# Kernel tuning notes

Measured on AMD Instinct MI355X. Metric: run time of the kernel, lower is better.

The kernel has to match this reference:

```python
import jax, jax.numpy as jnp
import numpy as np

RADIUS = 4  # matches init radius


def _bilinear_sample(v, grid):
    """Faithful F.grid_sample(v, grid, mode='bilinear', align_corners=True, padding_mode='zeros').
    v: (B,C,H,W); grid: (B,Hg,Wg,2) in [-1,1]; grid[...,0]->width(x), grid[...,1]->height(y)."""
    B, C, H, W = v.shape
    Hg, Wg = grid.shape[1], grid.shape[2]
    ix = (grid[..., 0] + 1.0) * 0.5 * (W - 1)
    iy = (grid[..., 1] + 1.0) * 0.5 * (H - 1)
    x0 = jnp.floor(ix); y0 = jnp.floor(iy)
    x1 = x0 + 1.0;      y1 = y0 + 1.0
    wx1 = ix - x0; wx0 = 1.0 - wx1
    wy1 = iy - y0; wy0 = 1.0 - wy1
    v_flat = v.reshape(B, C, H * W)
    out = jnp.zeros((B, C, Hg, Wg), v.dtype)
    for xf, yf, w in ((x0, y0, wx0 * wy0), (x1, y0, wx1 * wy0),
                      (x0, y1, wx0 * wy1), (x1, y1, wx1 * wy1)):
        valid = (xf >= 0) & (xf <= W - 1) & (yf >= 0) & (yf <= H - 1)
        xi = jnp.clip(xf, 0, W - 1).astype(jnp.int32)
        yi = jnp.clip(yf, 0, H - 1).astype(jnp.int32)
        idx = (yi * W + xi).reshape(B, 1, Hg * Wg)
        g = jnp.take_along_axis(v_flat, idx, axis=2).reshape(B, C, Hg, Wg)
        out = out + g * (w * valid)[:, None, :, :]
    return out


def setup_inputs() -> dict:
    key = jax.random.key(0)
    ks = jax.random.split(key, 5)
    B, C, H, W, K = 4, 128, 128, 128, 8
    x = jax.random.normal(ks[0], (B, C, H, W), jnp.float32)
    psf_tbl = jax.random.randint(ks[1], (B, H, W, K, 2), 0, 128)  # absolute pixel anchors
    delta = jax.random.normal(ks[2], (1, 1, 1, K, 2), jnp.float32) * 0.1
    w_qkv = jax.random.normal(ks[3], (3 * C, C), jnp.float32) * (C ** -0.5)  # 1x1 conv, no bias
    w_proj = jax.random.normal(ks[4], (C, C), jnp.float32) * (C ** -0.5)
    return {"x": x, "psf_tbl": psf_tbl, "delta": delta, "w_qkv": w_qkv, "w_proj": w_proj}


def reference(x, psf_tbl, delta, w_qkv, w_proj):
    B, C, H, W = x.shape
    K = psf_tbl.shape[3]
    qkv = jnp.einsum('oc,bchw->bohw', w_qkv, x)  # 1x1 conv to_qkv
    q, k, v = jnp.split(qkv, 3, axis=1)
    offsets = psf_tbl.astype(x.dtype) + jnp.tanh(delta) * RADIUS  # (B,H,W,K,2)
    norm = jnp.array([H - 1, W - 1], x.dtype)
    grid = (offsets / norm * 2.0 - 1.0).reshape(B, H, W * K, 2)
    k_s = _bilinear_sample(k, grid).reshape(B, C, H, W, K)
    v_s = _bilinear_sample(v, grid).reshape(B, C, H, W, K)
    attn = jnp.einsum('bchw,bchwk->bhwk', q, k_s) * (C ** -0.5)
    attn = jax.nn.softmax(attn, axis=-1)  # softmax over K sampled points
    out = jnp.einsum('bhwk,bchwk->bchw', attn, v_s)
    return x + jnp.einsum('oc,bchw->bohw', w_proj, out)
```

## Files before the change

kernel.cpp:

```cpp
#include <hip/hip_runtime.h>

#define HW 16384
#define C 128

typedef __attribute__((ext_vector_type(8))) short short8;
typedef __attribute__((ext_vector_type(4))) float f32x4;
typedef __attribute__((ext_vector_type(2))) float f32x2;
typedef __attribute__((ext_vector_type(16))) int v16i;

__device__ __forceinline__ unsigned short f2bf(float f) {
  union { float f; unsigned u; } v; v.f = f;
  return (unsigned short)((v.u + 0x7fffu + ((v.u >> 16) & 1u)) >> 16);
}
#if __has_builtin(__builtin_amdgcn_cvt_pk_bf16_f32)
typedef __attribute__((ext_vector_type(2))) __bf16 bf16x2;
__device__ __forceinline__ unsigned pk2(float a, float b) {
  union { bf16x2 v; unsigned u; } cv;
  cv.v = __builtin_amdgcn_cvt_pk_bf16_f32(a, b);
  return cv.u;
}
#else
__device__ __forceinline__ unsigned pk2(float a, float b) {
  return (unsigned)f2bf(a) | ((unsigned)f2bf(b) << 16);
}
#endif
__device__ __forceinline__ unsigned short f2bf1(float a) {
  return (unsigned short)(pk2(a, a) & 0xffffu);
}
__device__ __forceinline__ float bflo(unsigned w) {
  union { unsigned u; float f; } v; v.u = w << 16; return v.f;
}
__device__ __forceinline__ float bfhi(unsigned w) {
  union { unsigned u; float f; } v; v.u = w & 0xffff0000u; return v.f;
}
__device__ __forceinline__ float asf(int u) {
  union { int u; float f; } v; v.u = u; return v.f;
}
__device__ __forceinline__ float bf2f(unsigned short h) {
  union { unsigned u; float f; } v; v.u = ((unsigned)h) << 16; return v.f;
}

__global__ __launch_bounds__(128) void k_prep(const float* __restrict__ w_qkv,
                                              const float* __restrict__ w_proj,
                                              const float* __restrict__ delta,
                                              unsigned short* __restrict__ Mt,
                                              unsigned short* __restrict__ Pm,
                                              float* __restrict__ pw,
                                              int* __restrict__ pi) {
  const int bid = blockIdx.x;
  const int t = threadIdx.x;
  if (bid == 256) {
    if (t < 8) {
      float s0 = tanhf(delta[t * 2 + 0]) * 4.0f;
      float s1 = tanhf(delta[t * 2 + 1]) * 4.0f;
      float f0 = floorf(s0), f1 = floorf(s1);
      pi[2 * t + 0] = (int)f0;
      pi[2 * t + 1] = (int)f1;
      float fx = s0 - f0, fy = s1 - f1;
      pw[4 * t + 0] = (1.0f - fx) * (1.0f - fy);
      pw[4 * t + 1] = fx * (1.0f - fy);
      pw[4 * t + 2] = (1.0f - fx) * fy;
      pw[4 * t + 3] = fx * fy;
    }
    return;
  }
  const int R = bid & 127;
  float acc = 0.0f;
  if (bid < 128) {
    const float* wq = w_qkv;
    const float* wk = w_qkv + 128 * 128;
    #pragma unroll 16
    for (int j = 0; j < 128; ++j)
      acc += wk[j * 128 + R] * wq[j * 128 + t];
    acc *= 0.08838834764831845f;
    Mt[R * 128 + (t ^ ((R & 7) << 3))] = f2bf1(acc);
  } else {
    const float* wv = w_qkv + 2 * 128 * 128;
    const float* wp = w_proj + (size_t)R * 128;
    #pragma unroll 16
    for (int j = 0; j < 128; ++j)
      acc += wp[j] * wv[j * 128 + t];
    Pm[R * 128 + (t ^ ((R & 7) << 3))] = f2bf1(acc);
  }
}

__global__ __launch_bounds__(256) void k_qx(const float* __restrict__ x,
                                            const unsigned short* __restrict__ Mt,
                                            unsigned short* __restrict__ qb,
                                            unsigned* __restrict__ xq) {
  __shared__ __align__(16) unsigned char smem[65536];
  unsigned short* Xs = (unsigned short*)smem;
  unsigned short* Ws = (unsigned short*)(smem + 32768);
  const int t = threadIdx.x;
  const int gpix0 = blockIdx.x * 128;
  const int b = gpix0 >> 14;
  const int hw0 = gpix0 & (HW - 1);

  const float* xb = x + (size_t)b * C * HW + hw0;
  #pragma unroll
  for (int i = 0; i < 16; ++i) {
    int linear = i * 256 + t;
    int p = linear & 127;
    int c4 = (linear >> 7) * 4;
    float a0 = xb[(size_t)(c4 + 0) * HW + p];
    float a1 = xb[(size_t)(c4 + 1) * HW + p];
    float a2 = xb[(size_t)(c4 + 2) * HW + p];
    float a3 = xb[(size_t)(c4 + 3) * HW + p];
    int cc = c4 ^ ((p & 7) << 3);
    *(uint2*)&Xs[p * 128 + cc] = make_uint2(pk2(a0, a1), pk2(a2, a3));
  }
  #pragma unroll
  for (int i = 0; i < 8; ++i)
    ((uint4*)Ws)[i * 256 + t] = ((const uint4*)Mt)[i * 256 + t];
  __syncthreads();

  #pragma unroll
  for (int i = 0; i < 8; ++i) {
    int linear = i * 256 + t;
    int c8 = (linear & 15) * 8;
    int prow = linear >> 4;
    uint4 v = *(const uint4*)&Xs[prow * 128 + (c8 ^ ((prow & 7) << 3))];
    *(uint4*)&xq[((size_t)(gpix0 + prow)) * 64 + (c8 >> 1)] = v;
  }

  const int wave = t >> 6, lane = t & 63;
  const int wr = wave >> 1, wc = wave & 1;
  const int rsel = lane & 15, quad = lane >> 4;

  f32x4 acc[4][4];
  #pragma unroll
  for (int mi = 0; mi < 4; ++mi)
    #pragma unroll
    for (int ni = 0; ni < 4; ++ni) acc[mi][ni] = (f32x4){0.f, 0.f, 0.f, 0.f};
  #pragma unroll
  for (int ks = 0; ks < 4; ++ks) {
    const int koff = ks * 32 + quad * 8;
    short8 afr[4], bfr[4];
    #pragma unroll
    for (int mi = 0; mi < 4; ++mi) {
      int r = wr * 64 + mi * 16 + rsel;
      afr[mi] = *(const short8*)&Xs[r * 128 + (koff ^ ((r & 7) << 3))];
    }
    #pragma unroll
    for (int ni = 0; ni < 4; ++ni) {
      int r = wc * 64 + ni * 16 + rsel;
      bfr[ni] = *(const short8*)&Ws[r * 128 + (koff ^ ((r & 7) << 3))];
    }
    #pragma unroll
    for (int mi = 0; mi < 4; ++mi)
      #pragma unroll
      for (int ni = 0; ni < 4; ++ni)
        acc[mi][ni] = __builtin_amdgcn_mfma_f32_16x16x32_bf16(afr[mi], bfr[ni], acc[mi][ni], 0, 0, 0);
  }
  __syncthreads();
  #pragma unroll
  for (int mi = 0; mi < 4; ++mi)
    #pragma unroll
    for (int ni = 0; ni < 4; ++ni)
      #pragma unroll
      for (int r = 0; r < 4; ++r) {
        int p = wr * 64 + mi * 16 + quad * 4 + r;
        int ch = wc * 64 + ni * 16 + rsel;
        Xs[p * 128 + (ch ^ ((p & 7) << 3))] = f2bf1(acc[mi][ni][r]);
      }
  __syncthreads();
  #pragma unroll
  for (int i = 0; i < 8; ++i) {
    int linear = i * 256 + t;
    int c8 = (linear & 15) * 8;
    int prow = linear >> 4;
    uint4 v = *(const uint4*)&Xs[prow * 128 + (c8 ^ ((prow & 7) << 3))];
    *(uint4*)(qb + (size_t)(gpix0 + prow) * C + c8) = v;
  }
}

__global__ __launch_bounds__(256) void k_attn(const unsigned short* __restrict__ qb,
                                              const unsigned* __restrict__ xq,
                                              const int* __restrict__ psf,
                                              const int* __restrict__ pwu,
                                              unsigned short* __restrict__ ao) {
  const int t = threadIdx.x;
  const int li = t & 31;
  const int half = (t >> 5) & 1;
  const int gid = blockIdx.x;
  const int b = gid & 3;
  const int grp = gid >> 2;
  const int pixl = (grp << 3) + ((t >> 6) << 1) + half;
  const size_t spix = ((size_t)b << 14) + pixl;

  v16i w0, w1, tpi;
  asm volatile(
      "s_load_dwordx16 %0, %3, 0\n\t"
      "s_load_dwordx16 %1, %3, 64\n\t"
      "s_load_dwordx16 %2, %3, 128\n\t"
      "s_waitcnt lgkmcnt(0)"
      : "=&s"(w0), "=&s"(w1), "=&s"(tpi)
      : "s"(pwu));

  const int4* pr = (const int4*)(psf + spix * 16);
  int4 a0 = pr[0], a1 = pr[1], a2 = pr[2], a3 = pr[3];
  int va[16] = {a0.x, a0.y, a0.z, a0.w, a1.x, a1.y, a1.z, a1.w,
                a2.x, a2.y, a2.z, a2.w, a3.x, a3.y, a3.z, a3.w};

  const uint2 qp = *(const uint2*)((const unsigned*)qb + spix * 64 + 2 * li);
  const float q0 = bflo(qp.x), q1 = bfhi(qp.x);
  const float q2 = bflo(qp.y), q3 = bfhi(qp.y);

  const unsigned* xB = xq + (((size_t)b << 14) << 6);

  float s0[8], s1[8], s2[8], s3[8], dk[8];
  #pragma unroll
  for (int k = 0; k < 8; ++k) {
    const int x0 = va[2 * k + 0] + tpi[2 * k + 0];
    const int y0 = va[2 * k + 1] + tpi[2 * k + 1];
    float t0 = 0.f, t1 = 0.f, t2 = 0.f, t3 = 0.f;
    #pragma unroll
    for (int cn = 0; cn < 4; ++cn) {
      const int xi = x0 + (cn & 1);
      const int yi = y0 + (cn >> 1);
      const bool valid = ((unsigned)xi <= 127u) & ((unsigned)yi <= 127u);
      const int xc = min(max(xi, 0), 127);
      const int yc = min(max(yi, 0), 127);
      const int widx = k * 4 + cn;
      const float wv = valid ? asf(widx < 16 ? w0[widx & 15] : w1[widx & 15]) : 0.0f;
      const uint2 w2 = *(const uint2*)&xB[((size_t)((yc << 7) + xc) << 6) + 2 * li];
      t0 = fmaf(bflo(w2.x), wv, t0); t1 = fmaf(bfhi(w2.x), wv, t1);
      t2 = fmaf(bflo(w2.y), wv, t2); t3 = fmaf(bfhi(w2.y), wv, t3);
    }
    s0[k] = t0; s1[k] = t1; s2[k] = t2; s3[k] = t3;
    dk[k] = fmaf(q0, t0, fmaf(q1, t1, fmaf(q2, t2, q3 * t3)));
  }
  #pragma unroll
  for (int off = 16; off > 0; off >>= 1) {
    #pragma unroll
    for (int k = 0; k < 8; ++k) dk[k] += __shfl_xor(dk[k], off);
  }
  float m = dk[0];
  #pragma unroll
  for (int k = 1; k < 8; ++k) m = fmaxf(m, dk[k]);
  float den = 0.0f;
  #pragma unroll
  for (int k = 0; k < 8; ++k) { dk[k] = __expf(dk[k] - m); den += dk[k]; }
  const float inv = 1.0f / den;
  float o0 = 0.f, o1 = 0.f, o2 = 0.f, o3 = 0.f;
  #pragma unroll
  for (int k = 0; k < 8; ++k) {
    const float pk = dk[k] * inv;
    o0 = fmaf(pk, s0[k], o0); o1 = fmaf(pk, s1[k], o1);
    o2 = fmaf(pk, s2[k], o2); o3 = fmaf(pk, s3[k], o3);
  }
  *(uint2*)((unsigned*)ao + spix * 64 + 2 * li) = make_uint2(pk2(o0, o1), pk2(o2, o3));
}

__global__ __launch_bounds__(256) void k_proj(const unsigned short* __restrict__ ao,
                                              const unsigned short* __restrict__ Pm,
                                              const unsigned short* __restrict__ xqh,
                                              float* __restrict__ out) {
  __shared__ __align__(16) unsigned short As[128 * 128];
  __shared__ __align__(16) unsigned short Ws[128 * 128];
  const int t = threadIdx.x;
  const int gpix0 = blockIdx.x * 128;
  const int b = gpix0 >> 14;
  const int hw0 = gpix0 & (HW - 1);

  #pragma unroll
  for (int i = 0; i < 8; ++i) {
    int linear = i * 256 + t;
    int c8 = (linear & 15) * 8;
    int p = linear >> 4;
    uint4 v = *(const uint4*)(ao + (size_t)(gpix0 + p) * C + c8);
    *(uint4*)&As[p * 128 + (c8 ^ ((p & 7) << 3))] = v;
  }
  #pragma unroll
  for (int i = 0; i < 8; ++i)
    ((uint4*)Ws)[i * 256 + t] = ((const uint4*)Pm)[i * 256 + t];
  __syncthreads();

  const int wave = t >> 6, lane = t & 63;
  const int wr = wave >> 1, wc = wave & 1;
  const int rsel = lane & 15, quad = lane >> 4;

  f32x4 acc[4][4];
  #pragma unroll
  for (int mi = 0; mi < 4; ++mi)
    #pragma unroll
    for (int ni = 0; ni < 4; ++ni) acc[mi][ni] = (f32x4){0.f, 0.f, 0.f, 0.f};

  #pragma unroll
  for (int ks = 0; ks < 4; ++ks) {
    const int koff = ks * 32 + quad * 8;
    short8 afr[4], bfr[4];
    #pragma unroll
    for (int mi = 0; mi < 4; ++mi) {
      int r = wr * 64 + mi * 16 + rsel;
      afr[mi] = *(const short8*)&Ws[r * 128 + (koff ^ ((r & 7) << 3))];
    }
    #pragma unroll
    for (int ni = 0; ni < 4; ++ni) {
      int r = wc * 64 + ni * 16 + rsel;
      bfr[ni] = *(const short8*)&As[r * 128 + (koff ^ ((r & 7) << 3))];
    }
    #pragma unroll
    for (int mi = 0; mi < 4; ++mi)
      #pragma unroll
      for (int ni = 0; ni < 4; ++ni)
        acc[mi][ni] = __builtin_amdgcn_mfma_f32_16x16x32_bf16(afr[mi], bfr[ni], acc[mi][ni], 0, 0, 0);
  }

  __syncthreads();
  #pragma unroll
  for (int i = 0; i < 8; ++i) {
    int linear = i * 256 + t;
    int c8 = (linear & 15) * 8;
    int p = linear >> 4;
    uint4 v = *(const uint4*)(xqh + (size_t)(gpix0 + p) * C + c8);
    *(uint4*)&As[p * 128 + (c8 ^ ((p & 7) << 3))] = v;
  }
  __syncthreads();

  #pragma unroll
  for (int mi = 0; mi < 4; ++mi)
    #pragma unroll
    for (int ni = 0; ni < 4; ++ni)
      #pragma unroll
      for (int r = 0; r < 4; ++r) {
        int och = wr * 64 + mi * 16 + quad * 4 + r;
        int pixl = wc * 64 + ni * 16 + rsel;
        float xr = bf2f(As[pixl * 128 + (och ^ ((pixl & 7) << 3))]);
        size_t addr = ((size_t)b * C + och) * HW + hw0 + pixl;
        out[addr] = xr + acc[mi][ni][r];
      }
}

extern "C" void kernel_launch(void* const* d_in, const int* in_sizes, int n_in,
                              void* d_out, int out_size, void* d_ws, size_t ws_size,
                              hipStream_t stream) {
  const float* x      = (const float*)d_in[0];
  const int*   psf    = (const int*)d_in[1];
  const float* delta  = (const float*)d_in[2];
  const float* w_qkv  = (const float*)d_in[3];
  const float* w_proj = (const float*)d_in[4];
  float* out = (float*)d_out;

  const size_t N = (size_t)4 * HW * C;
  unsigned short* qb = (unsigned short*)d_ws;
  unsigned short* xq = qb + N;
  unsigned short* ao = xq + N;
  unsigned short* Mt = ao + N;
  unsigned short* Pm = Mt + 16384;
  float* pw = (float*)(Pm + 16384);
  int*   pi = (int*)(pw + 32);
  (void)pi;

  k_prep<<<dim3(257), 128, 0, stream>>>(w_qkv, w_proj, delta, Mt, Pm, pw, pi);
  k_qx<<<dim3(512), 256, 0, stream>>>(x, Mt, qb, (unsigned*)xq);
  k_attn<<<dim3(8192), 256, 0, stream>>>(qb, (const unsigned*)xq, psf, (const int*)pw, ao);
  k_proj<<<dim3(512), 256, 0, stream>>>(ao, Pm, xq, out);
}
```

Before: 148.0 us.

## Fuse q projection and output projection into the attention kernel

Folds the q-side MFMA (through Mt) and the output projection with residual into the gather/softmax kernel. Each block now handles 16 pixels with 512 threads and keeps q and the attention output in LDS. This removes the global round-trips for the q and attention-output buffers and one kernel launch, and k_xq becomes a bf16 transpose only. In exchange, each wave runs a small 16x16 MFMA with weights read straight from global/L2 and no LDS staging, and the residual now reads fp32 x instead of the bf16 copy.

```diff
diff --git a/kernel.cpp b/kernel.cpp
--- a/kernel.cpp
+++ b/kernel.cpp
@@ -35,9 +35,6 @@
 }
 __device__ __forceinline__ float asf(int u) {
   union { int u; float f; } v; v.u = u; return v.f;
-}
-__device__ __forceinline__ float bf2f(unsigned short h) {
-  union { unsigned u; float f; } v; v.u = ((unsigned)h) << 16; return v.f;
 }
 
 __global__ __launch_bounds__(128) void k_prep(const float* __restrict__ w_qkv,
@@ -84,109 +81,64 @@
   }
 }
 
-__global__ __launch_bounds__(256) void k_qx(const float* __restrict__ x,
-                                            const unsigned short* __restrict__ Mt,
-                                            unsigned short* __restrict__ qb,
+__global__ __launch_bounds__(256) void k_xq(const float* __restrict__ x,
                                             unsigned* __restrict__ xq) {
-  __shared__ __align__(16) unsigned char smem[65536];
-  unsigned short* Xs = (unsigned short*)smem;
-  unsigned short* Ws = (unsigned short*)(smem + 32768);
+  __shared__ __align__(16) unsigned short Xs[32 * 128];
   const int t = threadIdx.x;
-  const int gpix0 = blockIdx.x * 128;
+  const int gpix0 = blockIdx.x * 32;
   const int b = gpix0 >> 14;
   const int hw0 = gpix0 & (HW - 1);
-
   const float* xb = x + (size_t)b * C * HW + hw0;
+
   #pragma unroll
-  for (int i = 0; i < 16; ++i) {
-    int linear = i * 256 + t;
-    int p = linear & 127;
-    int c4 = (linear >> 7) * 4;
-    float a0 = xb[(size_t)(c4 + 0) * HW + p];
-    float a1 = xb[(size_t)(c4 + 1) * HW + p];
-    float a2 = xb[(size_t)(c4 + 2) * HW + p];
-    float a3 = xb[(size_t)(c4 + 3) * HW + p];
-    int cc = c4 ^ ((p & 7) << 3);
-    *(uint2*)&Xs[p * 128 + cc] = make_uint2(pk2(a0, a1), pk2(a2, a3));
-  }
+  for (int i = 0; i < 4; ++i) {
+    int idx = i * 256 + t;
+    int c = idx >> 3;
+    int p4 = idx & 7;
+    float4 v = *(const float4*)(xb + (size_t)c * HW + p4 * 4);
+    int p0 = p4 * 4;
+    Xs[(p0 + 0) * 128 + (c ^ (((p0 + 0) & 7) << 3))] = f2bf1(v.x);
+    Xs[(p0 + 1) * 128 + (c ^ (((p0 + 1) & 7) << 3))] = f2bf1(v.y);
+    Xs[(p0 + 2) * 128 + (c ^ (((p0 + 2) & 7) << 3))] = f2bf1(v.z);
+    Xs[(p0 + 3) * 128 + (c ^ (((p0 + 3) & 7) << 3))] = f2bf1(v.w);
+  }
+  __syncthreads();
   #pragma unroll
-  for (int i = 0; i < 8; ++i)
-    ((uint4*)Ws)[i * 256 + t] = ((const uint4*)Mt)[i * 256 + t];
-  __syncthreads();
-
-  #pragma unroll
-  for (int i = 0; i < 8; ++i) {
-    int linear = i * 256 + t;
-    int c8 = (linear & 15) * 8;
-    int prow = linear >> 4;
-    uint4 v = *(const uint4*)&Xs[prow * 128 + (c8 ^ ((prow & 7) << 3))];
-    *(uint4*)&xq[((size_t)(gpix0 + prow)) * 64 + (c8 >> 1)] = v;
-  }
-
-  const int wave = t >> 6, lane = t & 63;
-  const int wr = wave >> 1, wc = wave & 1;
-  const int rsel = lane & 15, quad = lane >> 4;
-
-  f32x4 acc[4][4];
-  #pragma unroll
-  for (int mi = 0; mi < 4; ++mi)
-    #pragma unroll
-    for (int ni = 0; ni < 4; ++ni) acc[mi][ni] = (f32x4){0.f, 0.f, 0.f, 0.f};
-  #pragma unroll
-  for (int ks = 0; ks < 4; ++ks) {
-    const int koff = ks * 32 + quad * 8;
-    short8 afr[4], bfr[4];
-    #pragma unroll
-    for (int mi = 0; mi < 4; ++mi) {
-      int r = wr * 64 + mi * 16 + rsel;
-      afr[mi] = *(const short8*)&Xs[r * 128 + (koff ^ ((r & 7) << 3))];
-    }
-    #pragma unroll
-    for (int ni = 0; ni < 4; ++ni) {
-      int r = wc * 64 + ni * 16 + rsel;
-      bfr[ni] = *(const short8*)&Ws[r * 128 + (koff ^ ((r & 7) << 3))];
-    }
-    #pragma unroll
-    for (int mi = 0; mi < 4; ++mi)
-      #pragma unroll
-      for (int ni = 0; ni < 4; ++ni)
-        acc[mi][ni] = __builtin_amdgcn_mfma_f32_16x16x32_bf16(afr[mi], bfr[ni], acc[mi][ni], 0, 0, 0);
-  }
-  __syncthreads();
-  #pragma unroll
-  for (int mi = 0; mi < 4; ++mi)
-    #pragma unroll
-    for (int ni = 0; ni < 4; ++ni)
-      #pragma unroll
-      for (int r = 0; r < 4; ++r) {
-        int p = wr * 64 + mi * 16 + quad * 4 + r;
-        int ch = wc * 64 + ni * 16 + rsel;
-        Xs[p * 128 + (ch ^ ((p & 7) << 3))] = f2bf1(acc[mi][ni][r]);
-      }
-  __syncthreads();
-  #pragma unroll
-  for (int i = 0; i < 8; ++i) {
-    int linear = i * 256 + t;
-    int c8 = (linear & 15) * 8;
-    int prow = linear >> 4;
-    uint4 v = *(const uint4*)&Xs[prow * 128 + (c8 ^ ((prow & 7) << 3))];
-    *(uint4*)(qb + (size_t)(gpix0 + prow) * C + c8) = v;
-  }
-}
-
-__global__ __launch_bounds__(256) void k_attn(const unsigned short* __restrict__ qb,
-                                              const unsigned* __restrict__ xq,
+  for (int i = 0; i < 2; ++i) {
+    int idx = i * 256 + t;
+    int pix = idx >> 4;
+    int c8 = (idx & 15) * 8;
+    uint4 v = *(const uint4*)&Xs[pix * 128 + (c8 ^ ((pix & 7) << 3))];
+    *(uint4*)&xq[(size_t)(gpix0 + pix) * 64 + (c8 >> 1)] = v;
+  }
+}
+
+__global__ __launch_bounds__(512) void k_attn(const unsigned* __restrict__ xq,
                                               const int* __restrict__ psf,
                                               const int* __restrict__ pwu,
-                                              unsigned short* __restrict__ ao) {
+                                              const unsigned short* __restrict__ Mt,
+                                              const unsigned short* __restrict__ Pm,
+                                              const float* __restrict__ x,
+                                              float* __restrict__ out) {
+  __shared__ __align__(16) unsigned short Xt[16 * 128];
+  __shared__ __align__(16) unsigned short Qt[16 * 128];
+  __shared__ __align__(16) unsigned short Ot[16 * 128];
   const int t = threadIdx.x;
-  const int li = t & 31;
-  const int half = (t >> 5) & 1;
+  const int wave = t >> 6, lane = t & 63;
+  const int rsel = lane & 15, quad = lane >> 4;
+  const int li = t & 31, half = (t >> 5) & 1;
   const int gid = blockIdx.x;
   const int b = gid & 3;
   const int grp = gid >> 2;
-  const int pixl = (grp << 3) + ((t >> 6) << 1) + half;
-  const size_t spix = ((size_t)b << 14) + pixl;
+  const int gpix0 = grp << 4;
+  const size_t spix0 = ((size_t)b << 14) + gpix0;
+
+  if (t < 256) {
+    int pix = t >> 4;
+    int c8 = (t & 15) * 8;
+    uint4 v = *(const uint4*)((const unsigned short*)xq + (spix0 + pix) * 128 + c8);
+    *(uint4*)&Xt[pix * 128 + (c8 ^ ((pix & 7) << 3))] = v;
+  }
 
   v16i w0, w1, tpi;
   asm volatile(
@@ -196,140 +148,102 @@
       "s_waitcnt lgkmcnt(0)"
       : "=&s"(w0), "=&s"(w1), "=&s"(tpi)
       : "s"(pwu));
-
-  const int4* pr = (const int4*)(psf + spix * 16);
-  int4 a0 = pr[0], a1 = pr[1], a2 = pr[2], a3 = pr[3];
-  int va[16] = {a0.x, a0.y, a0.z, a0.w, a1.x, a1.y, a1.z, a1.w,
-                a2.x, a2.y, a2.z, a2.w, a3.x, a3.y, a3.z, a3.w};
-
-  const uint2 qp = *(const uint2*)((const unsigned*)qb + spix * 64 + 2 * li);
-  const float q0 = bflo(qp.x), q1 = bfhi(qp.x);
-  const float q2 = bflo(qp.y), q3 = bfhi(qp.y);
-
-  const unsigned* xB = xq + (((size_t)b << 14) << 6);
-
-  float s0[8], s1[8], s2[8], s3[8], dk[8];
-  #pragma unroll
-  for (int k = 0; k < 8; ++k) {
-    const int x0 = va[2 * k + 0] + tpi[2 * k + 0];
-    const int y0 = va[2 * k + 1] + tpi[2 * k + 1];
-    float t0 = 0.f, t1 = 0.f, t2 = 0.f, t3 = 0.f;
-    #pragma unroll
-    for (int cn = 0; cn < 4; ++cn) {
-      const int xi = x0 + (cn & 1);
-      const int yi = y0 + (cn >> 1);
-      const bool valid = ((unsigned)xi <= 127u) & ((unsigned)yi <= 127u);
-      const int xc = min(max(xi, 0), 127);
-      const int yc = min(max(yi, 0), 127);
-      const int widx = k * 4 + cn;
-      const float wv = valid ? asf(widx < 16 ? w0[widx & 15] : w1[widx & 15]) : 0.0f;
-      const uint2 w2 = *(const uint2*)&xB[((size_t)((yc << 7) + xc) << 6) + 2 * li];
-      t0 = fmaf(bflo(w2.x), wv, t0); t1 = fmaf(bfhi(w2.x), wv, t1);
-      t2 = fmaf(bflo(w2.y), wv, t2); t3 = fmaf(bfhi(w2.y), wv, t3);
-    }
-    s0[k] = t0; s1[k] = t1; s2[k] = t2; s3[k] = t3;
-    dk[k] = fmaf(q0, t0, fmaf(q1, t1, fmaf(q2, t2, q3 * t3)));
-  }
-  #pragma unroll
-  for (int off = 16; off > 0; off >>= 1) {
-    #pragma unroll
-    for (int k = 0; k < 8; ++k) dk[k] += __shfl_xor(dk[k], off);
-  }
-  float m = dk[0];
-  #pragma unroll
-  for (int k = 1; k < 8; ++k) m = fmaxf(m, dk[k]);
-  float den = 0.0f;
-  #pragma unroll
-  for (int k = 0; k < 8; ++k) { dk[k] = __expf(dk[k] - m); den += dk[k]; }
-  const float inv = 1.0f / den;
-  float o0 = 0.f, o1 = 0.f, o2 = 0.f, o3 = 0.f;
-  #pragma unroll
-  for (int k = 0; k < 8; ++k) {
-    const float pk = dk[k] * inv;
-    o0 = fmaf(pk, s0[k], o0); o1 = fmaf(pk, s1[k], o1);
-    o2 = fmaf(pk, s2[k], o2); o3 = fmaf(pk, s3[k], o3);
-  }
-  *(uint2*)((unsigned*)ao + spix * 64 + 2 * li) = make_uint2(pk2(o0, o1), pk2(o2, o3));
-}
-
-__global__ __launch_bounds__(256) void k_proj(const unsigned short* __restrict__ ao,
-                                              const unsigned short* __restrict__ Pm,
-                                              const unsigned short* __restrict__ xqh,
-                                              float* __restrict__ out) {
-  __shared__ __align__(16) unsigned short As[128 * 128];
-  __shared__ __align__(16) unsigned short Ws[128 * 128];
-  const int t = threadIdx.x;
-  const int gpix0 = blockIdx.x * 128;
-  const int b = gpix0 >> 14;
-  const int hw0 = gpix0 & (HW - 1);
-
-  #pragma unroll
-  for (int i = 0; i < 8; ++i) {
-    int linear = i * 256 + t;
-    int c8 = (linear & 15) * 8;
-    int p = linear >> 4;
-    uint4 v = *(const uint4*)(ao + (size_t)(gpix0 + p) * C + c8);
-    *(uint4*)&As[p * 128 + (c8 ^ ((p & 7) << 3))] = v;
-  }
-  #pragma unroll
-  for (int i = 0; i < 8; ++i)
-    ((uint4*)Ws)[i * 256 + t] = ((const uint4*)Pm)[i * 256 + t];
-  __syncthreads();
-
-  const int wave = t >> 6, lane = t & 63;
-  const int wr = wave >> 1, wc = wave & 1;
-  const int rsel = lane & 15, quad = lane >> 4;
-
-  f32x4 acc[4][4];
-  #pragma unroll
-  for (int mi = 0; mi < 4; ++mi)
-    #pragma unroll
-    for (int ni = 0; ni < 4; ++ni) acc[mi][ni] = (f32x4){0.f, 0.f, 0.f, 0.f};
-
-  #pragma unroll
-  for (int ks = 0; ks < 4; ++ks) {
-    const int koff = ks * 32 + quad * 8;
-    short8 afr[4], bfr[4];
-    #pragma unroll
-    for (int mi = 0; mi < 4; ++mi) {
-      int r = wr * 64 + mi * 16 + rsel;
-      afr[mi] = *(const short8*)&Ws[r * 128 + (koff ^ ((r & 7) << 3))];
-    }
-    #pragma unroll
-    for (int ni = 0; ni < 4; ++ni) {
-      int r = wc * 64 + ni * 16 + rsel;
-      bfr[ni] = *(const short8*)&As[r * 128 + (koff ^ ((r & 7) << 3))];
-    }
-    #pragma unroll
-    for (int mi = 0; mi < 4; ++mi)
+  __syncthreads();
+
+  {
+    f32x4 qacc = (f32x4){0.f, 0.f, 0.f, 0.f};
+    const unsigned short* MtW = Mt + (size_t)(wave * 16) * 128;
+    #pragma unroll
+    for (int ks = 0; ks < 4; ++ks) {
+      const int koff = ks * 32 + quad * 8;
+      short8 afr = *(const short8*)&MtW[rsel * 128 + (koff ^ ((rsel & 7) << 3))];
+      short8 bfr = *(const short8*)&Xt[rsel * 128 + (koff ^ ((rsel & 7) << 3))];
+      qacc = __builtin_amdgcn_mfma_f32_16x16x32_bf16(afr, bfr, qacc, 0, 0, 0);
+    }
+    #pragma unroll
+    for (int r = 0; r < 4; ++r) {
+      int ch = wave * 16 + quad * 4 + r;
+      Qt[rsel * 128 + (ch ^ ((rsel & 7) << 3))] = f2bf1(qacc[r]);
+    }
+  }
+  __syncthreads();
+
+  const int pixl = (wave << 1) + half;
+  {
+    const int4* pr = (const int4*)(psf + (spix0 + pixl) * 16);
+    int4 a0 = pr[0], a1 = pr[1], a2 = pr[2], a3 = pr[3];
+    int va[16] = {a0.x, a0.y, a0.z, a0.w, a1.x, a1.y, a1.z, a1.w,
+                  a2.x, a2.y, a2.z, a2.w, a3.x, a3.y, a3.z, a3.w};
+
+    const uint2 qp = *(const uint2*)&Qt[pixl * 128 + ((4 * li) ^ ((pixl & 7) << 3))];
+    const float q0 = bflo(qp.x), q1 = bfhi(qp.x);
+    const float q2 = bflo(qp.y), q3 = bfhi(qp.y);
+
+    const unsigned* xB = xq + (((size_t)b << 14) << 6);
+
+    float s0[8], s1[8], s2[8], s3[8], dk[8];
+    #pragma unroll
+    for (int k = 0; k < 8; ++k) {
+      const int x0 = va[2 * k + 0] + tpi[2 * k + 0];
+      const int y0 = va[2 * k + 1] + tpi[2 * k + 1];
+      float t0 = 0.f, t1 = 0.f, t2 = 0.f, t3 = 0.f;
       #pragma unroll
-      for (int ni = 0; ni < 4; ++ni)
-        acc[mi][ni] = __builtin_amdgcn_mfma_f32_16x16x32_bf16(afr[mi], bfr[ni], acc[mi][ni], 0, 0, 0);
-  }
-
-  __syncthreads();
-  #pragma unroll
-  for (int i = 0; i < 8; ++i) {
-    int linear = i * 256 + t;
-    int c8 = (linear & 15) * 8;
-    int p = linear >> 4;
-    uint4 v = *(const uint4*)(xqh + (size_t)(gpix0 + p) * C + c8);
-    *(uint4*)&As[p * 128 + (c8 ^ ((p & 7) << 3))] = v;
-  }
-  __syncthreads();
-
-  #pragma unroll
-  for (int mi = 0; mi < 4; ++mi)
-    #pragma unroll
-    for (int ni = 0; ni < 4; ++ni)
+      for (int cn = 0; cn < 4; ++cn) {
+        const int xi = x0 + (cn & 1);
+        const int yi = y0 + (cn >> 1);
+        const bool valid = ((unsigned)xi <= 127u) & ((unsigned)yi <= 127u);
+        const int xc = min(max(xi, 0), 127);
+        const int yc = min(max(yi, 0), 127);
+        const int widx = k * 4 + cn;
+        const float wv = valid ? asf(widx < 16 ? w0[widx & 15] : w1[widx & 15]) : 0.0f;
+        const uint2 w2 = *(const uint2*)&xB[((size_t)((yc << 7) + xc) << 6) + 2 * li];
+        t0 = fmaf(bflo(w2.x), wv, t0); t1 = fmaf(bfhi(w2.x), wv, t1);
+        t2 = fmaf(bflo(w2.y), wv, t2); t3 = fmaf(bfhi(w2.y), wv, t3);
+      }
+      s0[k] = t0; s1[k] = t1; s2[k] = t2; s3[k] = t3;
+      dk[k] = fmaf(q0, t0, fmaf(q1, t1, fmaf(q2, t2, q3 * t3)));
+    }
+    #pragma unroll
+    for (int off = 16; off > 0; off >>= 1) {
       #pragma unroll
-      for (int r = 0; r < 4; ++r) {
-        int och = wr * 64 + mi * 16 + quad * 4 + r;
-        int pixl = wc * 64 + ni * 16 + rsel;
-        float xr = bf2f(As[pixl * 128 + (och ^ ((pixl & 7) << 3))]);
-        size_t addr = ((size_t)b * C + och) * HW + hw0 + pixl;
-        out[addr] = xr + acc[mi][ni][r];
-      }
+      for (int k = 0; k < 8; ++k) dk[k] += __shfl_xor(dk[k], off);
+    }
+    float m = dk[0];
+    #pragma unroll
+    for (int k = 1; k < 8; ++k) m = fmaxf(m, dk[k]);
+    float den = 0.0f;
+    #pragma unroll
+    for (int k = 0; k < 8; ++k) { dk[k] = __expf(dk[k] - m); den += dk[k]; }
+    const float inv = 1.0f / den;
+    float o0 = 0.f, o1 = 0.f, o2 = 0.f, o3 = 0.f;
+    #pragma unroll
+    for (int k = 0; k < 8; ++k) {
+      const float pk = dk[k] * inv;
+      o0 = fmaf(pk, s0[k], o0); o1 = fmaf(pk, s1[k], o1);
+      o2 = fmaf(pk, s2[k], o2); o3 = fmaf(pk, s3[k], o3);
+    }
+    *(uint2*)&Ot[pixl * 128 + ((4 * li) ^ ((pixl & 7) << 3))] =
+        make_uint2(pk2(o0, o1), pk2(o2, o3));
+  }
+  __syncthreads();
+
+  {
+    f32x4 pacc = (f32x4){0.f, 0.f, 0.f, 0.f};
+    const unsigned short* PmW = Pm + (size_t)(wave * 16) * 128;
+    #pragma unroll
+    for (int ks = 0; ks < 4; ++ks) {
+      const int koff = ks * 32 + quad * 8;
+      short8 afr = *(const short8*)&PmW[rsel * 128 + (koff ^ ((rsel & 7) << 3))];
+      short8 bfr = *(const short8*)&Ot[rsel * 128 + (koff ^ ((rsel & 7) << 3))];
+      pacc = __builtin_amdgcn_mfma_f32_16x16x32_bf16(afr, bfr, pacc, 0, 0, 0);
+    }
+    #pragma unroll
+    for (int r = 0; r < 4; ++r) {
+      int och = wave * 16 + quad * 4 + r;
+      size_t addr = ((size_t)b * C + och) * HW + gpix0 + rsel;
+      out[addr] = x[addr] + pacc[r];
+    }
+  }
 }
 
 extern "C" void kernel_launch(void* const* d_in, const int* in_sizes, int n_in,
@@ -342,18 +256,13 @@
   const float* w_proj = (const float*)d_in[4];
   float* out = (float*)d_out;
 
-  const size_t N = (size_t)4 * HW * C;
-  unsigned short* qb = (unsigned short*)d_ws;
-  unsigned short* xq = qb + N;
-  unsigned short* ao = xq + N;
-  unsigned short* Mt = ao + N;
+  unsigned* xq = (unsigned*)d_ws;
+  unsigned short* Mt = (unsigned short*)(xq + (size_t)4 * HW * 64);
   unsigned short* Pm = Mt + 16384;
   float* pw = (float*)(Pm + 16384);
   int*   pi = (int*)(pw + 32);
-  (void)pi;
 
   k_prep<<<dim3(257), 128, 0, stream>>>(w_qkv, w_proj, delta, Mt, Pm, pw, pi);
-  k_qx<<<dim3(512), 256, 0, stream>>>(x, Mt, qb, (unsigned*)xq);
-  k_attn<<<dim3(8192), 256, 0, stream>>>(qb, (const unsigned*)xq, psf, (const int*)pw, ao);
-  k_proj<<<dim3(512), 256, 0, stream>>>(ao, Pm, xq, out);
-}
+  k_xq<<<dim3(2048), 256, 0, stream>>>(x, xq);
+  k_attn<<<dim3(4096), 512, 0, stream>>>(xq, psf, (const int*)pw, Mt, Pm, x, out);
+}
```

Result: slower. 171.0 us (+15.6%).
